# Optimization experiments

Hardware: AMD Instinct MI355X
Metric: run time of the kernel (lower is better)

Reference implementation:

```python
import jax, jax.numpy as jnp
import numpy as np

TEMPERATURE = 100.0

def setup_inputs() -> dict:
    key = jax.random.key(0)
    n, d = 8192, 4096
    grad = jax.random.normal(key, (n, d), dtype=jnp.float32)
    return {"grad": grad}

def reference(grad) -> jnp.ndarray:
    # scores_i = sum_j (G @ G^T)_{ij} = G_i . (sum_j G_j)  -- avoids [n,n] gram
    colsum = jnp.sum(grad, axis=0)                 # [d]
    scores = grad @ colsum                         # [n]
    w = jax.nn.softmax(scores / TEMPERATURE, axis=0)  # softmax over rows (dim=0)
    # weighted row pooling: sum_i w_i * G_i -> [d]
    return w @ grad
```

## Files before the change

kernel.cpp:

```cpp
#include <hip/hip_runtime.h>
#include <math.h>

#define NROWS 8192
#define NCOLS 4096
#define NCOLS4 (NCOLS / 4)
#define TEMP_INV 0.01f

#define STRIPS 4
#define CHUNKS 512
#define CHUNK_ROWS (NROWS / CHUNKS)
#define STREAM_BLKS (STRIPS * CHUNKS)

__global__ __launch_bounds__(256)
void colsum_partial_kernel(const float* __restrict__ g,
                           float* __restrict__ partial) {
    const int strip = blockIdx.x & (STRIPS - 1);
    const int chunk = blockIdx.x >> 2;
    const int col   = strip * 1024 + threadIdx.x * 4;
    const float* p  = g + (size_t)chunk * CHUNK_ROWS * NCOLS + col;
    float4 acc = make_float4(0.f, 0.f, 0.f, 0.f);
    #pragma unroll
    for (int r = 0; r < CHUNK_ROWS; ++r) {
        float4 v = *reinterpret_cast<const float4*>(p);
        acc.x += v.x; acc.y += v.y; acc.z += v.z; acc.w += v.w;
        p += NCOLS;
    }
    *reinterpret_cast<float4*>(partial + (size_t)chunk * NCOLS + col) = acc;
}

__global__ __launch_bounds__(256)
void reduce_kernel(const float* __restrict__ partial, float* __restrict__ dst,
                   float* __restrict__ out) {
    const int tid = threadIdx.x;
    if (blockIdx.x < 4)
        reinterpret_cast<float4*>(out)[blockIdx.x * 256 + tid] =
            make_float4(0.f, 0.f, 0.f, 0.f);

    const int f4  = blockIdx.x * 16 + (tid & 15);
    const int grp = tid >> 4;
    const float4* p4 = reinterpret_cast<const float4*>(partial);
    float4 acc = make_float4(0.f, 0.f, 0.f, 0.f);
    #pragma unroll 8
    for (int c = grp; c < CHUNKS; c += 16) {
        float4 v = p4[(size_t)c * NCOLS4 + f4];
        acc.x += v.x; acc.y += v.y; acc.z += v.z; acc.w += v.w;
    }
    __shared__ float4 red[256];
    red[tid] = acc;
    __syncthreads();
    #pragma unroll
    for (int s = 128; s >= 16; s >>= 1) {
        if (tid < s) {
            float4 o = red[tid + s];
            red[tid].x += o.x; red[tid].y += o.y;
            red[tid].z += o.z; red[tid].w += o.w;
        }
        __syncthreads();
    }
    if (tid < 16)
        reinterpret_cast<float4*>(dst)[blockIdx.x * 16 + tid] = red[tid];
}

__global__ __launch_bounds__(256)
void scores_kernel(const float* __restrict__ g, const float* __restrict__ colsum,
                   float* __restrict__ scores) {
    __shared__ float4 cs4[NCOLS4];
    #pragma unroll
    for (int k = 0; k < NCOLS4 / 256; ++k)
        cs4[k * 256 + threadIdx.x] =
            reinterpret_cast<const float4*>(colsum)[k * 256 + threadIdx.x];
    __syncthreads();

    const int wave = threadIdx.x >> 6;
    const int lane = threadIdx.x & 63;
    const int row  = blockIdx.x * 4 + wave;
    const float4* gp = reinterpret_cast<const float4*>(g) + (size_t)row * NCOLS4;

    float4 acc = make_float4(0.f, 0.f, 0.f, 0.f);
    #pragma unroll
    for (int k = 0; k < 16; ++k) {
        const int idx = k * 64 + lane;
        float4 v = gp[idx];
        float4 c = cs4[idx];
        acc.x += v.x * c.x; acc.y += v.y * c.y;
        acc.z += v.z * c.z; acc.w += v.w * c.w;
    }
    float s = (acc.x + acc.y) + (acc.z + acc.w);
    #pragma unroll
    for (int off = 32; off; off >>= 1) s += __shfl_xor(s, off, 64);
    if (lane == 0) scores[row] = s;
}

__global__ __launch_bounds__(256)
void pool_kernel(const float* __restrict__ g, const float* __restrict__ scores,
                 float* __restrict__ out) {
    const int tid   = threadIdx.x;
    const int strip = blockIdx.x & (STRIPS - 1);
    const int chunk = blockIdx.x >> 2;
    const int wave  = tid >> 6;
    const int lane  = tid & 63;

    __shared__ float red[8];
    __shared__ float wsm[CHUNK_ROWS];

    const float4* s4 = reinterpret_cast<const float4*>(scores);
    float4 sv[8];
    float lm = -INFINITY;
    #pragma unroll
    for (int k = 0; k < 8; ++k) {
        sv[k] = s4[k * 256 + tid];
        lm = fmaxf(lm, fmaxf(fmaxf(sv[k].x, sv[k].y), fmaxf(sv[k].z, sv[k].w)));
    }
    #pragma unroll
    for (int off = 32; off; off >>= 1) lm = fmaxf(lm, __shfl_xor(lm, off, 64));
    if (lane == 0) red[wave] = lm;
    __syncthreads();
    const float m = fmaxf(fmaxf(red[0], red[1]), fmaxf(red[2], red[3]));

    float ls = 0.f;
    #pragma unroll
    for (int k = 0; k < 8; ++k) {
        ls += __expf((sv[k].x - m) * TEMP_INV)
            + __expf((sv[k].y - m) * TEMP_INV)
            + __expf((sv[k].z - m) * TEMP_INV)
            + __expf((sv[k].w - m) * TEMP_INV);
    }
    #pragma unroll
    for (int off = 32; off; off >>= 1) ls += __shfl_xor(ls, off, 64);
    if (lane == 0) red[4 + wave] = ls;
    __syncthreads();
    const float invZ = 1.0f / (red[4] + red[5] + red[6] + red[7]);

    if (tid < CHUNK_ROWS) {
        const float s = scores[chunk * CHUNK_ROWS + tid];
        wsm[tid] = __expf((s - m) * TEMP_INV) * invZ;
    }
    __syncthreads();

    const int col  = strip * 1024 + tid * 4;
    const float* p = g + (size_t)chunk * CHUNK_ROWS * NCOLS + col;
    float4 acc = make_float4(0.f, 0.f, 0.f, 0.f);
    #pragma unroll
    for (int r = 0; r < CHUNK_ROWS; ++r) {
        const float wt = wsm[r];
        float4 v = *reinterpret_cast<const float4*>(p);
        acc.x += wt * v.x; acc.y += wt * v.y;
        acc.z += wt * v.z; acc.w += wt * v.w;
        p += NCOLS;
    }
    atomicAdd(&out[col + 0], acc.x);
    atomicAdd(&out[col + 1], acc.y);
    atomicAdd(&out[col + 2], acc.z);
    atomicAdd(&out[col + 3], acc.w);
}

extern "C" void kernel_launch(void* const* d_in, const int* in_sizes, int n_in,
                              void* d_out, int out_size, void* d_ws, size_t ws_size,
                              hipStream_t stream) {
    const float* grad = (const float*)d_in[0];
    float* out = (float*)d_out;

    float* partial = (float*)d_ws;
    float* colsum  = partial + (size_t)CHUNKS * NCOLS;
    float* scores  = colsum + NCOLS;

    colsum_partial_kernel<<<STREAM_BLKS, 256, 0, stream>>>(grad, partial);
    reduce_kernel<<<64, 256, 0, stream>>>(partial, colsum, out);
    scores_kernel<<<NROWS / 4, 256, 0, stream>>>(grad, colsum, scores);
    pool_kernel<<<STREAM_BLKS, 256, 0, stream>>>(grad, scores, out);
}
```

Baseline: 279.1 us.

## Fuse scores and pooling into one online-softmax pass over grad

```diff
diff --git a/kernel.cpp b/kernel.cpp
--- a/kernel.cpp
+++ b/kernel.cpp
@@ -7,9 +7,19 @@
 #define TEMP_INV 0.01f
 
 #define STRIPS 4
-#define CHUNKS 512
-#define CHUNK_ROWS (NROWS / CHUNKS)
-#define STREAM_BLKS (STRIPS * CHUNKS)
+#define CS_CHUNKS 256
+#define CS_ROWS (NROWS / CS_CHUNKS)
+#define CS_BLKS (STRIPS * CS_CHUNKS)
+
+#define FB 512
+#define WPB 4
+#define NWAVE (FB * WPB)
+#define RPW (NROWS / NWAVE)
+#define KPL (NCOLS4 / 64)
+
+#define WGRP 16
+#define WPG (NWAVE / WGRP)
+#define CGRP 4
 
 __global__ __launch_bounds__(256)
 void colsum_partial_kernel(const float* __restrict__ g,
@@ -17,10 +27,10 @@
     const int strip = blockIdx.x & (STRIPS - 1);
     const int chunk = blockIdx.x >> 2;
     const int col   = strip * 1024 + threadIdx.x * 4;
-    const float* p  = g + (size_t)chunk * CHUNK_ROWS * NCOLS + col;
+    const float* p  = g + (size_t)chunk * CS_ROWS * NCOLS + col;
     float4 acc = make_float4(0.f, 0.f, 0.f, 0.f);
     #pragma unroll
-    for (int r = 0; r < CHUNK_ROWS; ++r) {
+    for (int r = 0; r < CS_ROWS; ++r) {
         float4 v = *reinterpret_cast<const float4*>(p);
         acc.x += v.x; acc.y += v.y; acc.z += v.z; acc.w += v.w;
         p += NCOLS;
@@ -40,8 +50,8 @@
     const int grp = tid >> 4;
     const float4* p4 = reinterpret_cast<const float4*>(partial);
     float4 acc = make_float4(0.f, 0.f, 0.f, 0.f);
-    #pragma unroll 8
-    for (int c = grp; c < CHUNKS; c += 16) {
+    #pragma unroll 4
+    for (int c = grp; c < CS_CHUNKS; c += 16) {
         float4 v = p4[(size_t)c * NCOLS4 + f4];
         acc.x += v.x; acc.y += v.y; acc.z += v.z; acc.w += v.w;
     }
@@ -62,96 +72,107 @@
 }
 
 __global__ __launch_bounds__(256)
-void scores_kernel(const float* __restrict__ g, const float* __restrict__ colsum,
-                   float* __restrict__ scores) {
+void fused_kernel(const float* __restrict__ g, const float* __restrict__ colsum,
+                  float* __restrict__ pnum, float2* __restrict__ mz) {
     __shared__ float4 cs4[NCOLS4];
-    #pragma unroll
-    for (int k = 0; k < NCOLS4 / 256; ++k)
-        cs4[k * 256 + threadIdx.x] =
-            reinterpret_cast<const float4*>(colsum)[k * 256 + threadIdx.x];
+    for (int k = threadIdx.x; k < NCOLS4; k += 256)
+        cs4[k] = reinterpret_cast<const float4*>(colsum)[k];
     __syncthreads();
 
     const int wave = threadIdx.x >> 6;
     const int lane = threadIdx.x & 63;
-    const int row  = blockIdx.x * 4 + wave;
-    const float4* gp = reinterpret_cast<const float4*>(g) + (size_t)row * NCOLS4;
+    const int wid  = blockIdx.x * WPB + wave;
 
-    float4 acc = make_float4(0.f, 0.f, 0.f, 0.f);
+    float4 acc[KPL];
     #pragma unroll
-    for (int k = 0; k < 16; ++k) {
-        const int idx = k * 64 + lane;
-        float4 v = gp[idx];
-        float4 c = cs4[idx];
-        acc.x += v.x * c.x; acc.y += v.y * c.y;
-        acc.z += v.z * c.z; acc.w += v.w * c.w;
+    for (int k = 0; k < KPL; ++k) acc[k] = make_float4(0.f, 0.f, 0.f, 0.f);
+    float m = -INFINITY, Z = 0.f;
+
+    #pragma unroll
+    for (int r = 0; r < RPW; ++r) {
+        const int row = wid * RPW + r;
+        const float4* rp = reinterpret_cast<const float4*>(g)
+                         + (size_t)row * NCOLS4;
+        float4 v[KPL];
+        float4 d = make_float4(0.f, 0.f, 0.f, 0.f);
+        #pragma unroll
+        for (int k = 0; k < KPL; ++k) {
+            v[k] = rp[k * 64 + lane];
+            float4 c = cs4[k * 64 + lane];
+            d.x += v[k].x * c.x; d.y += v[k].y * c.y;
+            d.z += v[k].z * c.z; d.w += v[k].w * c.w;
+        }
+        float s = (d.x + d.y) + (d.z + d.w);
+        #pragma unroll
+        for (int off = 32; off; off >>= 1) s += __shfl_xor(s, off, 64);
+
+        const float mnew  = fmaxf(m, s);
+        const float scale = (m == -INFINITY) ? 0.f
+                          : __expf((m - mnew) * TEMP_INV);
+        const float e     = __expf((s - mnew) * TEMP_INV);
+        Z = Z * scale + e;
+        #pragma unroll
+        for (int k = 0; k < KPL; ++k) {
+            acc[k].x = acc[k].x * scale + e * v[k].x;
+            acc[k].y = acc[k].y * scale + e * v[k].y;
+            acc[k].z = acc[k].z * scale + e * v[k].z;
+            acc[k].w = acc[k].w * scale + e * v[k].w;
+        }
+        m = mnew;
     }
-    float s = (acc.x + acc.y) + (acc.z + acc.w);
+
+    float4* pp = reinterpret_cast<float4*>(pnum) + (size_t)wid * NCOLS4;
     #pragma unroll
-    for (int off = 32; off; off >>= 1) s += __shfl_xor(s, off, 64);
-    if (lane == 0) scores[row] = s;
+    for (int k = 0; k < KPL; ++k) pp[k * 64 + lane] = acc[k];
+    if (lane == 0) mz[wid] = make_float2(m, Z);
 }
 
 __global__ __launch_bounds__(256)
-void pool_kernel(const float* __restrict__ g, const float* __restrict__ scores,
-                 float* __restrict__ out) {
-    const int tid   = threadIdx.x;
-    const int strip = blockIdx.x & (STRIPS - 1);
-    const int chunk = blockIdx.x >> 2;
-    const int wave  = tid >> 6;
-    const int lane  = tid & 63;
+void combine_kernel(const float* __restrict__ pnum, const float2* __restrict__ mz,
+                    float* __restrict__ out) {
+    __shared__ float red[8];
+    __shared__ float fsh[WPG];
+    const int tid = threadIdx.x;
+    const int wg  = blockIdx.x >> 2;
+    const int cg  = blockIdx.x & 3;
+    const int wave = tid >> 6, lane = tid & 63;
 
-    __shared__ float red[8];
-    __shared__ float wsm[CHUNK_ROWS];
-
-    const float4* s4 = reinterpret_cast<const float4*>(scores);
-    float4 sv[8];
     float lm = -INFINITY;
-    #pragma unroll
-    for (int k = 0; k < 8; ++k) {
-        sv[k] = s4[k * 256 + tid];
-        lm = fmaxf(lm, fmaxf(fmaxf(sv[k].x, sv[k].y), fmaxf(sv[k].z, sv[k].w)));
-    }
+    for (int i = tid; i < NWAVE; i += 256) lm = fmaxf(lm, mz[i].x);
     #pragma unroll
     for (int off = 32; off; off >>= 1) lm = fmaxf(lm, __shfl_xor(lm, off, 64));
     if (lane == 0) red[wave] = lm;
     __syncthreads();
-    const float m = fmaxf(fmaxf(red[0], red[1]), fmaxf(red[2], red[3]));
+    const float M = fmaxf(fmaxf(red[0], red[1]), fmaxf(red[2], red[3]));
 
-    float ls = 0.f;
+    float lz = 0.f;
+    for (int i = tid; i < NWAVE; i += 256)
+        lz += mz[i].y * __expf((mz[i].x - M) * TEMP_INV);
     #pragma unroll
-    for (int k = 0; k < 8; ++k) {
-        ls += __expf((sv[k].x - m) * TEMP_INV)
-            + __expf((sv[k].y - m) * TEMP_INV)
-            + __expf((sv[k].z - m) * TEMP_INV)
-            + __expf((sv[k].w - m) * TEMP_INV);
-    }
-    #pragma unroll
-    for (int off = 32; off; off >>= 1) ls += __shfl_xor(ls, off, 64);
-    if (lane == 0) red[4 + wave] = ls;
+    for (int off = 32; off; off >>= 1) lz += __shfl_xor(lz, off, 64);
+    if (lane == 0) red[4 + wave] = lz;
     __syncthreads();
     const float invZ = 1.0f / (red[4] + red[5] + red[6] + red[7]);
 
-    if (tid < CHUNK_ROWS) {
-        const float s = scores[chunk * CHUNK_ROWS + tid];
-        wsm[tid] = __expf((s - m) * TEMP_INV) * invZ;
+    if (tid < WPG) {
+        const int w = wg * WPG + tid;
+        fsh[tid] = __expf((mz[w].x - M) * TEMP_INV) * invZ;
     }
     __syncthreads();
 
-    const int col  = strip * 1024 + tid * 4;
-    const float* p = g + (size_t)chunk * CHUNK_ROWS * NCOLS + col;
-    float4 acc = make_float4(0.f, 0.f, 0.f, 0.f);
-    #pragma unroll
-    for (int r = 0; r < CHUNK_ROWS; ++r) {
-        const float wt = wsm[r];
-        float4 v = *reinterpret_cast<const float4*>(p);
-        acc.x += wt * v.x; acc.y += wt * v.y;
-        acc.z += wt * v.z; acc.w += wt * v.w;
-        p += NCOLS;
+    const int col4 = cg * 256 + tid;
+    float4 a = make_float4(0.f, 0.f, 0.f, 0.f);
+    const float4* p4 = reinterpret_cast<const float4*>(pnum);
+    #pragma unroll 4
+    for (int w = 0; w < WPG; ++w) {
+        float4 v = p4[(size_t)(wg * WPG + w) * NCOLS4 + col4];
+        const float f = fsh[w];
+        a.x += f * v.x; a.y += f * v.y; a.z += f * v.z; a.w += f * v.w;
     }
-    atomicAdd(&out[col + 0], acc.x);
-    atomicAdd(&out[col + 1], acc.y);
-    atomicAdd(&out[col + 2], acc.z);
-    atomicAdd(&out[col + 3], acc.w);
+    atomicAdd(&out[col4 * 4 + 0], a.x);
+    atomicAdd(&out[col4 * 4 + 1], a.y);
+    atomicAdd(&out[col4 * 4 + 2], a.z);
+    atomicAdd(&out[col4 * 4 + 3], a.w);
 }
 
 extern "C" void kernel_launch(void* const* d_in, const int* in_sizes, int n_in,
@@ -160,12 +181,13 @@
     const float* grad = (const float*)d_in[0];
     float* out = (float*)d_out;
 
-    float* partial = (float*)d_ws;
-    float* colsum  = partial + (size_t)CHUNKS * NCOLS;
-    float* scores  = colsum + NCOLS;
+    float* pcs    = (float*)d_ws;
+    float* colsum = pcs + (size_t)CS_CHUNKS * NCOLS;
+    float* pnum   = colsum + NCOLS;
+    float2* mz    = (float2*)(pnum + (size_t)NWAVE * NCOLS);
 
-    colsum_partial_kernel<<<STREAM_BLKS, 256, 0, stream>>>(grad, partial);
-    reduce_kernel<<<64, 256, 0, stream>>>(partial, colsum, out);
-    scores_kernel<<<NROWS / 4, 256, 0, stream>>>(grad, colsum, scores);
-    pool_kernel<<<STREAM_BLKS, 256, 0, stream>>>(grad, scores, out);
+    colsum_partial_kernel<<<CS_BLKS, 256, 0, stream>>>(grad, pcs);
+    reduce_kernel<<<64, 256, 0, stream>>>(pcs, colsum, out);
+    fused_kernel<<<FB, 256, 0, stream>>>(grad, colsum, pnum, mz);
+    combine_kernel<<<64, 256, 0, stream>>>(pnum, mz, out);
 }
```

Result: faster. 236.7 us (-15.2%).
